# Performance work log

Hardware: AMD Instinct MI355X
Metric: run time of the kernel (lower is better)

Reference implementation:

```python
import jax, jax.numpy as jnp
import numpy as np

B, V, E, H, L = 1024, 8192, 64, 64, 16
TAU = 1.2
SOS_ID, EOS_ID = 1, 2


def setup_inputs() -> dict:
    key = jax.random.key(0)
    ks = jax.random.split(key, 7)
    hidden_state = jax.random.normal(ks[0], (B, H), dtype=jnp.float32)
    # embedding ~ N(0, 0.1) as in reset_parameters
    embedding = 0.1 * jax.random.normal(ks[1], (V, E), dtype=jnp.float32)
    # LSTMCell weight_ih: xavier uniform, weight_hh: orthogonal
    bound = float(np.sqrt(6.0 / (4 * H + E)))
    W_ih = jax.random.uniform(ks[2], (4 * H, E), minval=-bound, maxval=bound, dtype=jnp.float32)
    a = jax.random.normal(ks[3], (4 * H, H), dtype=jnp.float32)
    q, r = jnp.linalg.qr(a)
    W_hh = q * jnp.sign(jnp.diagonal(r))  # [4H, H] orthogonal columns
    b_ih = jnp.zeros((4 * H,), jnp.float32)
    b_hh = jnp.zeros((4 * H,), jnp.float32).at[H:2 * H].set(1.0)  # forget-gate bias = 1
    # linear_out is zero-init in the torch code; use small random values so the
    # math under test is non-trivial (init is data, not math).
    W_out = 0.02 * jax.random.normal(ks[4], (V, H), dtype=jnp.float32)
    b_out = jnp.zeros((V,), jnp.float32)
    # Precomputed standard Gumbel noise for deterministic sampling
    u = jax.random.uniform(ks[5], (L, B, V), minval=1e-10, maxval=1.0, dtype=jnp.float32)
    gumbels = -jnp.log(-jnp.log(u))
    return {
        'hidden_state': hidden_state, 'embedding': embedding,
        'W_ih': W_ih, 'W_hh': W_hh, 'b_ih': b_ih, 'b_hh': b_hh,
        'W_out': W_out, 'b_out': b_out, 'gumbels': gumbels,
    }


def reference(hidden_state, embedding, W_ih, W_hh, b_ih, b_hh, W_out, b_out, gumbels):
    b, h_dim = hidden_state.shape
    v = embedding.shape[0]
    n_steps = gumbels.shape[0]
    initial_length = n_steps + 1

    sos_onehot = jnp.zeros((b, v), hidden_state.dtype).at[:, SOS_ID].set(1.0)

    def step(carry, xs):
        h, c, prev_token, seq_lengths, ent = carry
        g, i = xs
        emb = prev_token @ embedding                                   # [b, E]
        gates = emb @ W_ih.T + b_ih + h @ W_hh.T + b_hh                # [b, 4H]
        ii, ff, gg, oo = jnp.split(gates, 4, axis=-1)                  # torch order i,f,g,o
        c = jax.nn.sigmoid(ff) * c + jax.nn.sigmoid(ii) * jnp.tanh(gg)
        h = jax.nn.sigmoid(oo) * jnp.tanh(c)
        logits = h @ W_out.T + b_out                                   # [b, V]
        logp = jax.nn.log_softmax(logits, axis=-1)
        p = jnp.exp(logp)
        ent = ent - jnp.sum(p * logp, axis=-1)
        # RelaxedOneHotCategorical rsample: softmax((log p + gumbel) / tau)
        y = jax.nn.softmax((logp + g) / TAU, axis=-1)
        y_hard = jax.nn.one_hot(jnp.argmax(y, axis=-1), v, dtype=y.dtype)
        token = jax.lax.stop_gradient(y_hard - y) + y                  # straight-through
        max_pred = jnp.max(token, axis=-1)
        vocab_idx = jnp.argmax(token, axis=-1)
        mask = (vocab_idx == EOS_ID) & (max_pred == 1.0) & (seq_lengths == initial_length)
        seq_lengths = jnp.where(mask, i + 2, seq_lengths)              # seq_pos + 1 with seq_pos = i+1
        return (h, c, token, seq_lengths, ent), (token, emb)

    c0 = jnp.zeros_like(hidden_state)
    seq0 = jnp.full((b,), initial_length, jnp.int32)
    ent0 = jnp.zeros((b,), hidden_state.dtype)
    (_, _, _, seq_lengths, ent), (tokens, embeds) = jax.lax.scan(
        step, (hidden_state, c0, sos_onehot, seq0, ent0),
        (gumbels, jnp.arange(n_steps, dtype=jnp.int32)))

    output = jnp.concatenate([sos_onehot[:, None, :], jnp.swapaxes(tokens, 0, 1)], axis=1)  # [b, L+1, V]
    embeds = jnp.swapaxes(embeds, 0, 1)                                                      # [b, L, E]
    entropy = jnp.mean(ent) / n_steps
    return output, seq_lengths, entropy, hidden_state, embeds
```

## Files before the change

kernel.cpp:

```cpp
#include <hip/hip_runtime.h>
#include <cmath>

#define B_ 1024
#define V_ 8192
#define E_ 64
#define H_ 64
#define L_ 16
#define SOS 1
#define EOS 2

typedef float f32x4 __attribute__((ext_vector_type(4)));

#define ONEHOT_OFF 0ull
#define SEQ_OFF    142606336ull
#define ENT_OFF    142607360ull
#define HID_OFF    142607361ull
#define EMB_OFF    142672897ull

__global__ __launch_bounds__(256) void init_zero_kernel(float* __restrict__ out)
{
    const int t = threadIdx.x;
    const int row = blockIdx.x;
    float* slab = out + ONEHOT_OFF + (size_t)row * (17 * 8192);
#pragma unroll
    for (int j = 0; j < 8; ++j) {
        f32x4 z = {0.f, 0.f, 0.f, 0.f};
        if (j == 0 && t == 0) z.y = 1.0f;
        __builtin_nontemporal_store(z, (f32x4*)(slab + j * 1024 + t * 4));
    }
    if (row == 0 && t == 1) out[ENT_OFF] = 0.f;
}

__global__ __launch_bounds__(256, 2) void logits_stats_kernel(
    const float* __restrict__ Wout, const float* __restrict__ bout,
    const float* __restrict__ gstep,
    const float* __restrict__ h,
    float* __restrict__ pm, float* __restrict__ pS, float* __restrict__ pT,
    float* __restrict__ pbv, int* __restrict__ pbi,
    float* __restrict__ out, int step)
{
    __shared__ float wV[256][64];
    __shared__ float hV[16][68];

    const int t  = threadIdx.x;
    const int rg = blockIdx.x >> 3;
    const int vs = blockIdx.x & 7;
    const int rowBase = rg * 16;
    const int tv = t & 63;
    const int tr = t >> 6;
    const int r0 = tr * 4;

    const int srow = t >> 4;
    const int scc  = t & 15;
    const int sdst = ((scc ^ srow) << 2);

    {
        const int rl = t >> 4;
        const int k0 = (t & 15) * 4;
        float4 hv = *(const float4*)(h + (size_t)(rowBase + rl) * 64 + k0);
        *(float4*)&hV[rl][k0] = hv;
    }

    {
        const f32x4 z = {0.f, 0.f, 0.f, 0.f};
        const size_t slab = ONEHOT_OFF + (size_t)(step + 1) * 8192 + (size_t)(vs * 1024 + t * 4);
#pragma unroll
        for (int r = 0; r < 16; ++r) {
            __builtin_nontemporal_store(z,
                (f32x4*)(out + (size_t)(rowBase + r) * (17 * 8192) + slab));
        }
    }

    float m[4], S[4], T[4], bv[4];
    int   bi[4];
#pragma unroll
    for (int r = 0; r < 4; ++r) {
        m[r] = -INFINITY; S[r] = 0.f; T[r] = 0.f; bv[r] = -INFINITY; bi[r] = 0;
    }

    for (int cc = 0; cc < 4; ++cc) {
        const int vglob = vs * 1024 + cc * 256;

        float gv[16], bo[4];
#pragma unroll
        for (int j = 0; j < 4; ++j) {
            const int v = vglob + 64 * j + tv;
            bo[j] = bout[v];
#pragma unroll
            for (int r = 0; r < 4; ++r)
                gv[j * 4 + r] = gstep[(size_t)(rowBase + r0 + r) * V_ + v];
        }

        __syncthreads();
#pragma unroll
        for (int j = 0; j < 16; ++j) {
            const int vl = srow + 16 * j;
            float4 w = *(const float4*)(Wout + (size_t)(vglob + vl) * 64 + scc * 4);
            *(float4*)&wV[vl][sdst] = w;
        }
        __syncthreads();

        float acc[4][4];
#pragma unroll
        for (int r = 0; r < 4; ++r)
#pragma unroll
            for (int j = 0; j < 4; ++j) acc[r][j] = 0.f;

#pragma unroll 4
        for (int k4 = 0; k4 < 16; ++k4) {
            const int ks = ((k4 ^ (tv & 15)) << 2);
            float4 wv[4], hv[4];
#pragma unroll
            for (int j = 0; j < 4; ++j) wv[j] = *(const float4*)&wV[tv + 64 * j][ks];
#pragma unroll
            for (int r = 0; r < 4; ++r) hv[r] = *(const float4*)&hV[r0 + r][k4 * 4];
#pragma unroll
            for (int r = 0; r < 4; ++r)
#pragma unroll
                for (int j = 0; j < 4; ++j)
                    acc[r][j] += hv[r].x * wv[j].x + hv[r].y * wv[j].y +
                                 hv[r].z * wv[j].z + hv[r].w * wv[j].w;
        }

#pragma unroll
        for (int j = 0; j < 4; ++j) {
            const int v  = vglob + 64 * j + tv;
#pragma unroll
            for (int r = 0; r < 4; ++r) {
                const float l = acc[r][j] + bo[j];
                const float s = l + gv[j * 4 + r];
                if (s > bv[r]) { bv[r] = s; bi[r] = v; }
                const float mn = fmaxf(m[r], l);
                const float e  = __expf(-fabsf(l - m[r]));
                const bool nw  = l > m[r];
                const float a  = nw ? e : 1.f;
                const float b2 = nw ? 1.f : e;
                S[r] = S[r] * a + b2;
                T[r] = T[r] * a + l * b2;
                m[r] = mn;
            }
        }
    }

#pragma unroll
    for (int off = 1; off < 64; off <<= 1) {
#pragma unroll
        for (int r = 0; r < 4; ++r) {
            const float mo  = __shfl_xor(m[r], off);
            const float So  = __shfl_xor(S[r], off);
            const float To  = __shfl_xor(T[r], off);
            const float bvo = __shfl_xor(bv[r], off);
            const int   bio = __shfl_xor(bi[r], off);
            const float mn = fmaxf(m[r], mo);
            const float ea = __expf(m[r] - mn);
            const float eb = __expf(mo - mn);
            S[r] = S[r] * ea + So * eb;
            T[r] = T[r] * ea + To * eb;
            m[r] = mn;
            if (bvo > bv[r] || (bvo == bv[r] && bio < bi[r])) { bv[r] = bvo; bi[r] = bio; }
        }
    }
    if (tv == 0) {
#pragma unroll
        for (int r = 0; r < 4; ++r) {
            const int row = rowBase + r0 + r;
            const int o = vs * 1024 + row;
            pm[o] = m[r]; pS[o] = S[r]; pT[o] = T[r]; pbv[o] = bv[r]; pbi[o] = bi[r];
        }
    }
}

__global__ __launch_bounds__(256) void combine_lstm_kernel(
    const float* __restrict__ emb_table,
    const float* __restrict__ W_ih, const float* __restrict__ W_hh,
    const float* __restrict__ b_ih, const float* __restrict__ b_hh,
    const float* __restrict__ hidden_in,
    float* __restrict__ h, float* __restrict__ c,
    float* __restrict__ ent, int* __restrict__ seq,
    const float* __restrict__ pm, const float* __restrict__ pS,
    const float* __restrict__ pT, const float* __restrict__ pbv,
    const int* __restrict__ pbi,
    float* __restrict__ out, int step)
{
    __shared__ float wrow[256][132];
    __shared__ float xcat[8][128];
    __shared__ float gatesL[8][256];
    __shared__ int   toksL[8];
    __shared__ float entL[8];

    const int t = threadIdx.x;
    const int rowBase = blockIdx.x * 8;

    if (step >= 0) {
        if (t < 8) {
            const int row = rowBase + t;
            float m = -INFINITY, S = 0.f, T = 0.f, bv = -INFINITY; int bi = 0;
            for (int s = 0; s < 8; ++s) {
                const int o = s * 1024 + row;
                const float ms = pm[o], Ss = pS[o], Ts = pT[o], bvs = pbv[o];
                const int bis = pbi[o];
                const float mn = fmaxf(m, ms);
                const float ea = __expf(m - mn), eb = __expf(ms - mn);
                S = S * ea + Ss * eb; T = T * ea + Ts * eb; m = mn;
                if (bvs > bv || (bvs == bv && bis < bi)) { bv = bvs; bi = bis; }
            }
            const float lse  = m + logf(S);
            const float entc = lse - T / S;
            const int tok = bi;
            out[ONEHOT_OFF + (size_t)row * (17 * 8192) + (size_t)(step + 1) * 8192 + tok] = 1.0f;
            const float ev = (step == 0) ? entc : (ent[row] + entc);
            ent[row] = ev;
            int sl = (step == 0) ? (L_ + 1) : seq[row];
            if (tok == EOS && sl == (L_ + 1)) sl = step + 2;
            seq[row] = sl;
            toksL[t] = tok;
            entL[t] = ev;
            if (step == 15) out[SEQ_OFF + row] = (float)sl;
        }
    } else {
        if (t < 8) toksL[t] = SOS;
    }
    __syncthreads();

    if (step == 15) {
        if (t == 0) {
            float a = 0.f;
            for (int r = 0; r < 8; ++r) a += entL[r];
            atomicAdd(out + ENT_OFF, a * (1.0f / (1024.0f * 16.0f)));
        }
        return;
    }

#pragma unroll
    for (int j = 0; j < 16; ++j) {
        const int f  = (t + 256 * j) * 4;
        const int gr = f >> 6;
        const int k0 = f & 63;
        *(float4*)&wrow[gr][k0]      = *(const float4*)(W_ih + f);
        *(float4*)&wrow[gr][64 + k0] = *(const float4*)(W_hh + f);
    }
    if (t < 128) {
        const int r = t >> 4, k0 = (t & 15) * 4;
        const int row = rowBase + r;
        const int tk = (step < 0) ? SOS : toksL[r];
        float4 evv = *(const float4*)(emb_table + (size_t)tk * 64 + k0);
        *(float4*)&xcat[r][k0] = evv;
        const size_t eo = EMB_OFF + ((size_t)row * 16 + (size_t)(step + 1)) * 64 + k0;
        out[eo + 0] = evv.x; out[eo + 1] = evv.y; out[eo + 2] = evv.z; out[eo + 3] = evv.w;
    } else {
        const int tt = t - 128;
        const int r = tt >> 4, k0 = (tt & 15) * 4;
        const int row = rowBase + r;
        const float* hsrc = (step < 0) ? (hidden_in + (size_t)row * 64 + k0)
                                       : (h + (size_t)row * 64 + k0);
        float4 hv = *(const float4*)hsrc;
        *(float4*)&xcat[r][64 + k0] = hv;
    }
    __syncthreads();

    {
        const float bia = b_ih[t] + b_hh[t];
        float acc[8];
#pragma unroll
        for (int r = 0; r < 8; ++r) acc[r] = bia;
        for (int k4 = 0; k4 < 32; ++k4) {
            const float4 w4 = *(const float4*)&wrow[t][k4 * 4];
#pragma unroll
            for (int r = 0; r < 8; ++r) {
                const float4 x4 = *(const float4*)&xcat[r][k4 * 4];
                acc[r] += x4.x * w4.x + x4.y * w4.y + x4.z * w4.z + x4.w * w4.w;
            }
        }
#pragma unroll
        for (int r = 0; r < 8; ++r) gatesL[r][t] = acc[r];
    }
    __syncthreads();

#pragma unroll
    for (int q = 0; q < 2; ++q) {
        const int u = t + q * 256;
        const int r = u >> 6, uu = u & 63;
        const int row = rowBase + r;
        const float ii = gatesL[r][uu];
        const float ff = gatesL[r][64 + uu];
        const float gg = gatesL[r][128 + uu];
        const float oo = gatesL[r][192 + uu];
        const float cp = (step < 0) ? 0.f : c[(size_t)row * 64 + uu];
        const float si = 1.f / (1.f + expf(-ii));
        const float sf = 1.f / (1.f + expf(-ff));
        const float so = 1.f / (1.f + expf(-oo));
        const float cn = sf * cp + si * tanhf(gg);
        const float hn = so * tanhf(cn);
        c[(size_t)row * 64 + uu] = cn;
        h[(size_t)row * 64 + uu] = hn;
    }
}

extern "C" void kernel_launch(void* const* d_in, const int* in_sizes, int n_in,
                              void* d_out, int out_size, void* d_ws, size_t ws_size,
                              hipStream_t stream) {
    (void)in_sizes; (void)ws_size; (void)out_size;
    if (n_in < 9) return;
    const float* hidden    = (const float*)d_in[0];
    const float* embedding = (const float*)d_in[1];
    const float* W_ih      = (const float*)d_in[2];
    const float* W_hh      = (const float*)d_in[3];
    const float* b_ih      = (const float*)d_in[4];
    const float* b_hh      = (const float*)d_in[5];
    const float* W_out     = (const float*)d_in[6];
    const float* b_out     = (const float*)d_in[7];
    const float* gumbels   = (const float*)d_in[8];
    float* out = (float*)d_out;

    float* wsf = (float*)d_ws;
    float* h   = wsf;
    float* c   = wsf + 65536;
    float* ent = wsf + 131072;
    int*   seq = (int*)(wsf + 132096);
    float* pm  = wsf + 133120;
    float* pS  = pm + 8192;
    float* pT  = pS + 8192;
    float* pbv = pT + 8192;
    int*   pbi = (int*)(pbv + 8192);

    (void)hipMemcpyAsync(out + HID_OFF, hidden, (size_t)B_ * H_ * sizeof(float),
                         hipMemcpyDeviceToDevice, stream);
    init_zero_kernel<<<1024, 256, 0, stream>>>(out);

    combine_lstm_kernel<<<128, 256, 0, stream>>>(embedding, W_ih, W_hh, b_ih, b_hh,
        hidden, h, c, ent, seq, pm, pS, pT, pbv, pbi, out, -1);
    for (int i = 0; i < 16; ++i) {
        logits_stats_kernel<<<512, 256, 0, stream>>>(W_out, b_out,
            gumbels + (size_t)i * B_ * V_, h, pm, pS, pT, pbv, pbi, out, i);
        combine_lstm_kernel<<<128, 256, 0, stream>>>(embedding, W_ih, W_hh, b_ih, b_hh,
            hidden, h, c, ent, seq, pm, pS, pT, pbv, pbi, out, i);
    }
}
```

Measured before the change: 1.543 ms.

## Fuse all decode steps into one persistent kernel with per-row-group flag barriers

Replaces the 33 per-step launches (logits/stats plus combine/LSTM) with a single persistent kernel of 512 blocks. The eight blocks covering a 16-row group synchronise through atomic flag counters in global memory. The LSTM gate computation is split across those eight blocks by hidden unit, with the cell state kept in registers and h exchanged through a workspace buffer. This removes launch gaps and the h/c round trips, but it depends on all 512 blocks being co-resident, since the spin barriers would deadlock otherwise, and it adds spin-wait overhead.

```diff
diff --git a/kernel.cpp b/kernel.cpp
--- a/kernel.cpp
+++ b/kernel.cpp
@@ -17,7 +17,8 @@
 #define HID_OFF    142607361ull
 #define EMB_OFF    142672897ull
 
-__global__ __launch_bounds__(256) void init_zero_kernel(float* __restrict__ out)
+__global__ __launch_bounds__(256) void init_zero_kernel(float* __restrict__ out,
+                                                        int* __restrict__ flags)
 {
     const int t = threadIdx.x;
     const int row = blockIdx.x;
@@ -29,18 +30,30 @@
         __builtin_nontemporal_store(z, (f32x4*)(slab + j * 1024 + t * 4));
     }
     if (row == 0 && t == 1) out[ENT_OFF] = 0.f;
+    if (row == 1) flags[t] = 0;
+    if (row == 2) flags[256 + t] = 0;
+    if (row == 3) flags[512 + t] = 0;
+    if (row == 4) flags[768 + t] = 0;
 }
 
-__global__ __launch_bounds__(256, 2) void logits_stats_kernel(
+__global__ __launch_bounds__(256, 2) void fused_kernel(
+    const float* __restrict__ emb_table,
+    const float* __restrict__ W_ih, const float* __restrict__ W_hh,
+    const float* __restrict__ b_ih, const float* __restrict__ b_hh,
+    const float* __restrict__ hidden_in,
     const float* __restrict__ Wout, const float* __restrict__ bout,
-    const float* __restrict__ gstep,
-    const float* __restrict__ h,
+    const float* __restrict__ gumbels,
     float* __restrict__ pm, float* __restrict__ pS, float* __restrict__ pT,
     float* __restrict__ pbv, int* __restrict__ pbi,
-    float* __restrict__ out, int step)
+    float* __restrict__ hx,
+    int* __restrict__ flags,
+    float* __restrict__ out)
 {
     __shared__ float wV[256][64];
-    __shared__ float hV[16][68];
+    __shared__ float X[16][132];
+    __shared__ int   tokL[16];
+    __shared__ float entL[16];
+    __shared__ int   seqL[16];
 
     const int t  = threadIdx.x;
     const int rg = blockIdx.x >> 3;
@@ -54,245 +67,249 @@
     const int scc  = t & 15;
     const int sdst = ((scc ^ srow) << 2);
 
+    float c_reg = 0.f;
+    int sync_ev = 0;
+
+    auto rg_sync = [&]() {
+        __syncthreads();
+        ++sync_ev;
+        if (t == 0) {
+            __hip_atomic_fetch_add(&flags[rg * 16], 1, __ATOMIC_RELEASE,
+                                   __HIP_MEMORY_SCOPE_AGENT);
+            while (__hip_atomic_load(&flags[rg * 16], __ATOMIC_ACQUIRE,
+                                     __HIP_MEMORY_SCOPE_AGENT) < 8 * sync_ev)
+                __builtin_amdgcn_s_sleep(2);
+        }
+        __syncthreads();
+    };
+
+    auto gates_lstm = [&]() {
+        float* Wg = &wV[0][0];
+#pragma unroll
+        for (int q = 0; q < 4; ++q) {
+            const int idx = (q * 256 + t) * 4;
+            const int gr = idx >> 7;
+            const int k  = idx & 127;
+            const int g = gr >> 3, ul = gr & 7;
+            const int wrow = g * 64 + vs * 8 + ul;
+            const float* src = (k < 64) ? (W_ih + (size_t)wrow * 64 + k)
+                                        : (W_hh + (size_t)wrow * 64 + (k - 64));
+            *(float4*)(Wg + gr * 128 + k) = *(const float4*)src;
+        }
+        __syncthreads();
+        if (t < 128) {
+            const int row = t >> 3, ul = t & 7;
+            const int unit = vs * 8 + ul;
+            float a0 = b_ih[unit]       + b_hh[unit];
+            float a1 = b_ih[64 + unit]  + b_hh[64 + unit];
+            float a2 = b_ih[128 + unit] + b_hh[128 + unit];
+            float a3 = b_ih[192 + unit] + b_hh[192 + unit];
+            for (int k4 = 0; k4 < 32; ++k4) {
+                const float4 x4 = *(const float4*)&X[row][k4 * 4];
+                const float4 w0 = *(const float4*)(Wg + (0 * 8 + ul) * 128 + k4 * 4);
+                const float4 w1 = *(const float4*)(Wg + (1 * 8 + ul) * 128 + k4 * 4);
+                const float4 w2 = *(const float4*)(Wg + (2 * 8 + ul) * 128 + k4 * 4);
+                const float4 w3 = *(const float4*)(Wg + (3 * 8 + ul) * 128 + k4 * 4);
+                a0 += x4.x * w0.x + x4.y * w0.y + x4.z * w0.z + x4.w * w0.w;
+                a1 += x4.x * w1.x + x4.y * w1.y + x4.z * w1.z + x4.w * w1.w;
+                a2 += x4.x * w2.x + x4.y * w2.y + x4.z * w2.z + x4.w * w2.w;
+                a3 += x4.x * w3.x + x4.y * w3.y + x4.z * w3.z + x4.w * w3.w;
+            }
+            const float si = 1.f / (1.f + expf(-a0));
+            const float sf = 1.f / (1.f + expf(-a1));
+            const float so = 1.f / (1.f + expf(-a3));
+            const float cn = sf * c_reg + si * tanhf(a2);
+            const float hn = so * tanhf(cn);
+            c_reg = cn;
+            hx[((size_t)(rg * 8 + vs) * 16 + row) * 8 + ul] = hn;
+        }
+        rg_sync();
+        {
+            const int row = t >> 4, k0 = (t & 15) * 4;
+            const int vsp = k0 >> 3, off = k0 & 7;
+            float4 hv = *(const float4*)(hx + ((size_t)(rg * 8 + vsp) * 16 + row) * 8 + off);
+            *(float4*)&X[row][64 + k0] = hv;
+        }
+        __syncthreads();
+    };
+
     {
-        const int rl = t >> 4;
-        const int k0 = (t & 15) * 4;
-        float4 hv = *(const float4*)(h + (size_t)(rowBase + rl) * 64 + k0);
-        *(float4*)&hV[rl][k0] = hv;
+        const int row = t >> 4, k0 = (t & 15) * 4;
+        float4 evv = *(const float4*)(emb_table + (size_t)SOS * 64 + k0);
+        *(float4*)&X[row][k0] = evv;
+        if (vs == 0) {
+            const size_t eo = EMB_OFF + ((size_t)(rowBase + row) * 16 + 0) * 64 + k0;
+            out[eo + 0] = evv.x; out[eo + 1] = evv.y; out[eo + 2] = evv.z; out[eo + 3] = evv.w;
+        }
+        float4 hv = *(const float4*)(hidden_in + (size_t)(rowBase + row) * 64 + k0);
+        *(float4*)&X[row][64 + k0] = hv;
     }
-
-    {
-        const f32x4 z = {0.f, 0.f, 0.f, 0.f};
-        const size_t slab = ONEHOT_OFF + (size_t)(step + 1) * 8192 + (size_t)(vs * 1024 + t * 4);
-#pragma unroll
-        for (int r = 0; r < 16; ++r) {
-            __builtin_nontemporal_store(z,
-                (f32x4*)(out + (size_t)(rowBase + r) * (17 * 8192) + slab));
-        }
-    }
-
-    float m[4], S[4], T[4], bv[4];
-    int   bi[4];
-#pragma unroll
-    for (int r = 0; r < 4; ++r) {
-        m[r] = -INFINITY; S[r] = 0.f; T[r] = 0.f; bv[r] = -INFINITY; bi[r] = 0;
-    }
-
-    for (int cc = 0; cc < 4; ++cc) {
-        const int vglob = vs * 1024 + cc * 256;
-
-        float gv[16], bo[4];
-#pragma unroll
-        for (int j = 0; j < 4; ++j) {
-            const int v = vglob + 64 * j + tv;
-            bo[j] = bout[v];
+    __syncthreads();
+    gates_lstm();
+
+    for (int i = 0; i < 16; ++i) {
+        const float* gstep = gumbels + (size_t)i * 8388608ull;
+
+        {
+            const f32x4 z = {0.f, 0.f, 0.f, 0.f};
+            const size_t slab = ONEHOT_OFF + (size_t)(i + 1) * 8192 + (size_t)(vs * 1024 + t * 4);
+#pragma unroll
+            for (int r = 0; r < 16; ++r) {
+                __builtin_nontemporal_store(z,
+                    (f32x4*)(out + (size_t)(rowBase + r) * (17 * 8192) + slab));
+            }
+        }
+
+        float m[4], S[4], T[4], bv[4];
+        int   bi[4];
+#pragma unroll
+        for (int r = 0; r < 4; ++r) {
+            m[r] = -INFINITY; S[r] = 0.f; T[r] = 0.f; bv[r] = -INFINITY; bi[r] = 0;
+        }
+
+        for (int cc = 0; cc < 4; ++cc) {
+            const int vglob = vs * 1024 + cc * 256;
+
+            float gv[16], bo[4];
+#pragma unroll
+            for (int j = 0; j < 4; ++j) {
+                const int v = vglob + 64 * j + tv;
+                bo[j] = bout[v];
+#pragma unroll
+                for (int r = 0; r < 4; ++r)
+                    gv[j * 4 + r] = gstep[(size_t)(rowBase + r0 + r) * V_ + v];
+            }
+
+            __syncthreads();
+#pragma unroll
+            for (int j = 0; j < 16; ++j) {
+                const int vl = srow + 16 * j;
+                float4 w = *(const float4*)(Wout + (size_t)(vglob + vl) * 64 + scc * 4);
+                *(float4*)&wV[vl][sdst] = w;
+            }
+            __syncthreads();
+
+            float acc[4][4];
 #pragma unroll
             for (int r = 0; r < 4; ++r)
-                gv[j * 4 + r] = gstep[(size_t)(rowBase + r0 + r) * V_ + v];
-        }
-
-        __syncthreads();
-#pragma unroll
-        for (int j = 0; j < 16; ++j) {
-            const int vl = srow + 16 * j;
-            float4 w = *(const float4*)(Wout + (size_t)(vglob + vl) * 64 + scc * 4);
-            *(float4*)&wV[vl][sdst] = w;
-        }
-        __syncthreads();
-
-        float acc[4][4];
-#pragma unroll
-        for (int r = 0; r < 4; ++r)
-#pragma unroll
-            for (int j = 0; j < 4; ++j) acc[r][j] = 0.f;
+#pragma unroll
+                for (int j = 0; j < 4; ++j) acc[r][j] = 0.f;
 
 #pragma unroll 4
-        for (int k4 = 0; k4 < 16; ++k4) {
-            const int ks = ((k4 ^ (tv & 15)) << 2);
-            float4 wv[4], hv[4];
-#pragma unroll
-            for (int j = 0; j < 4; ++j) wv[j] = *(const float4*)&wV[tv + 64 * j][ks];
-#pragma unroll
-            for (int r = 0; r < 4; ++r) hv[r] = *(const float4*)&hV[r0 + r][k4 * 4];
-#pragma unroll
-            for (int r = 0; r < 4; ++r)
-#pragma unroll
-                for (int j = 0; j < 4; ++j)
-                    acc[r][j] += hv[r].x * wv[j].x + hv[r].y * wv[j].y +
-                                 hv[r].z * wv[j].z + hv[r].w * wv[j].w;
-        }
-
-#pragma unroll
-        for (int j = 0; j < 4; ++j) {
-            const int v  = vglob + 64 * j + tv;
+            for (int k4 = 0; k4 < 16; ++k4) {
+                const int ks = ((k4 ^ (tv & 15)) << 2);
+                float4 wv[4], hv[4];
+#pragma unroll
+                for (int j = 0; j < 4; ++j) wv[j] = *(const float4*)&wV[tv + 64 * j][ks];
+#pragma unroll
+                for (int r = 0; r < 4; ++r) hv[r] = *(const float4*)&X[r0 + r][64 + k4 * 4];
+#pragma unroll
+                for (int r = 0; r < 4; ++r)
+#pragma unroll
+                    for (int j = 0; j < 4; ++j)
+                        acc[r][j] += hv[r].x * wv[j].x + hv[r].y * wv[j].y +
+                                     hv[r].z * wv[j].z + hv[r].w * wv[j].w;
+            }
+
+#pragma unroll
+            for (int j = 0; j < 4; ++j) {
+                const int v  = vglob + 64 * j + tv;
+#pragma unroll
+                for (int r = 0; r < 4; ++r) {
+                    const float l = acc[r][j] + bo[j];
+                    const float s = l + gv[j * 4 + r];
+                    if (s > bv[r]) { bv[r] = s; bi[r] = v; }
+                    const float mn = fmaxf(m[r], l);
+                    const float e  = __expf(-fabsf(l - m[r]));
+                    const bool nw  = l > m[r];
+                    const float a  = nw ? e : 1.f;
+                    const float b2 = nw ? 1.f : e;
+                    S[r] = S[r] * a + b2;
+                    T[r] = T[r] * a + l * b2;
+                    m[r] = mn;
+                }
+            }
+        }
+
+#pragma unroll
+        for (int off = 1; off < 64; off <<= 1) {
 #pragma unroll
             for (int r = 0; r < 4; ++r) {
-                const float l = acc[r][j] + bo[j];
-                const float s = l + gv[j * 4 + r];
-                if (s > bv[r]) { bv[r] = s; bi[r] = v; }
-                const float mn = fmaxf(m[r], l);
-                const float e  = __expf(-fabsf(l - m[r]));
-                const bool nw  = l > m[r];
-                const float a  = nw ? e : 1.f;
-                const float b2 = nw ? 1.f : e;
-                S[r] = S[r] * a + b2;
-                T[r] = T[r] * a + l * b2;
+                const float mo  = __shfl_xor(m[r], off);
+                const float So  = __shfl_xor(S[r], off);
+                const float To  = __shfl_xor(T[r], off);
+                const float bvo = __shfl_xor(bv[r], off);
+                const int   bio = __shfl_xor(bi[r], off);
+                const float mn = fmaxf(m[r], mo);
+                const float ea = __expf(m[r] - mn);
+                const float eb = __expf(mo - mn);
+                S[r] = S[r] * ea + So * eb;
+                T[r] = T[r] * ea + To * eb;
                 m[r] = mn;
-            }
-        }
-    }
-
-#pragma unroll
-    for (int off = 1; off < 64; off <<= 1) {
-#pragma unroll
-        for (int r = 0; r < 4; ++r) {
-            const float mo  = __shfl_xor(m[r], off);
-            const float So  = __shfl_xor(S[r], off);
-            const float To  = __shfl_xor(T[r], off);
-            const float bvo = __shfl_xor(bv[r], off);
-            const int   bio = __shfl_xor(bi[r], off);
-            const float mn = fmaxf(m[r], mo);
-            const float ea = __expf(m[r] - mn);
-            const float eb = __expf(mo - mn);
-            S[r] = S[r] * ea + So * eb;
-            T[r] = T[r] * ea + To * eb;
-            m[r] = mn;
-            if (bvo > bv[r] || (bvo == bv[r] && bio < bi[r])) { bv[r] = bvo; bi[r] = bio; }
-        }
-    }
-    if (tv == 0) {
-#pragma unroll
-        for (int r = 0; r < 4; ++r) {
-            const int row = rowBase + r0 + r;
-            const int o = vs * 1024 + row;
-            pm[o] = m[r]; pS[o] = S[r]; pT[o] = T[r]; pbv[o] = bv[r]; pbi[o] = bi[r];
-        }
-    }
-}
-
-__global__ __launch_bounds__(256) void combine_lstm_kernel(
-    const float* __restrict__ emb_table,
-    const float* __restrict__ W_ih, const float* __restrict__ W_hh,
-    const float* __restrict__ b_ih, const float* __restrict__ b_hh,
-    const float* __restrict__ hidden_in,
-    float* __restrict__ h, float* __restrict__ c,
-    float* __restrict__ ent, int* __restrict__ seq,
-    const float* __restrict__ pm, const float* __restrict__ pS,
-    const float* __restrict__ pT, const float* __restrict__ pbv,
-    const int* __restrict__ pbi,
-    float* __restrict__ out, int step)
-{
-    __shared__ float wrow[256][132];
-    __shared__ float xcat[8][128];
-    __shared__ float gatesL[8][256];
-    __shared__ int   toksL[8];
-    __shared__ float entL[8];
-
-    const int t = threadIdx.x;
-    const int rowBase = blockIdx.x * 8;
-
-    if (step >= 0) {
-        if (t < 8) {
+                if (bvo > bv[r] || (bvo == bv[r] && bio < bi[r])) { bv[r] = bvo; bi[r] = bio; }
+            }
+        }
+        if (tv == 0) {
+#pragma unroll
+            for (int r = 0; r < 4; ++r) {
+                const int row = rowBase + r0 + r;
+                const int o = vs * 1024 + row;
+                pm[o] = m[r]; pS[o] = S[r]; pT[o] = T[r]; pbv[o] = bv[r]; pbi[o] = bi[r];
+            }
+        }
+        rg_sync();
+
+        if (t < 16) {
             const int row = rowBase + t;
-            float m = -INFINITY, S = 0.f, T = 0.f, bv = -INFINITY; int bi = 0;
+            float m2 = -INFINITY, S2 = 0.f, T2 = 0.f, bv2 = -INFINITY; int bi2 = 0;
             for (int s = 0; s < 8; ++s) {
                 const int o = s * 1024 + row;
                 const float ms = pm[o], Ss = pS[o], Ts = pT[o], bvs = pbv[o];
                 const int bis = pbi[o];
-                const float mn = fmaxf(m, ms);
-                const float ea = __expf(m - mn), eb = __expf(ms - mn);
-                S = S * ea + Ss * eb; T = T * ea + Ts * eb; m = mn;
-                if (bvs > bv || (bvs == bv && bis < bi)) { bv = bvs; bi = bis; }
-            }
-            const float lse  = m + logf(S);
-            const float entc = lse - T / S;
-            const int tok = bi;
-            out[ONEHOT_OFF + (size_t)row * (17 * 8192) + (size_t)(step + 1) * 8192 + tok] = 1.0f;
-            const float ev = (step == 0) ? entc : (ent[row] + entc);
-            ent[row] = ev;
-            int sl = (step == 0) ? (L_ + 1) : seq[row];
-            if (tok == EOS && sl == (L_ + 1)) sl = step + 2;
-            seq[row] = sl;
-            toksL[t] = tok;
+                const float mn = fmaxf(m2, ms);
+                const float ea = __expf(m2 - mn), eb = __expf(ms - mn);
+                S2 = S2 * ea + Ss * eb; T2 = T2 * ea + Ts * eb; m2 = mn;
+                if (bvs > bv2 || (bvs == bv2 && bis < bi2)) { bv2 = bvs; bi2 = bis; }
+            }
+            const float lse  = m2 + logf(S2);
+            const float entc = lse - T2 / S2;
+            const int tok = bi2;
+            if (vs == 0)
+                out[ONEHOT_OFF + (size_t)row * (17 * 8192) + (size_t)(i + 1) * 8192 + tok] = 1.0f;
+            const float ev = (i == 0) ? entc : (entL[t] + entc);
             entL[t] = ev;
-            if (step == 15) out[SEQ_OFF + row] = (float)sl;
-        }
-    } else {
-        if (t < 8) toksL[t] = SOS;
-    }
-    __syncthreads();
-
-    if (step == 15) {
-        if (t == 0) {
-            float a = 0.f;
-            for (int r = 0; r < 8; ++r) a += entL[r];
-            atomicAdd(out + ENT_OFF, a * (1.0f / (1024.0f * 16.0f)));
-        }
-        return;
-    }
-
-#pragma unroll
-    for (int j = 0; j < 16; ++j) {
-        const int f  = (t + 256 * j) * 4;
-        const int gr = f >> 6;
-        const int k0 = f & 63;
-        *(float4*)&wrow[gr][k0]      = *(const float4*)(W_ih + f);
-        *(float4*)&wrow[gr][64 + k0] = *(const float4*)(W_hh + f);
-    }
-    if (t < 128) {
-        const int r = t >> 4, k0 = (t & 15) * 4;
-        const int row = rowBase + r;
-        const int tk = (step < 0) ? SOS : toksL[r];
-        float4 evv = *(const float4*)(emb_table + (size_t)tk * 64 + k0);
-        *(float4*)&xcat[r][k0] = evv;
-        const size_t eo = EMB_OFF + ((size_t)row * 16 + (size_t)(step + 1)) * 64 + k0;
-        out[eo + 0] = evv.x; out[eo + 1] = evv.y; out[eo + 2] = evv.z; out[eo + 3] = evv.w;
-    } else {
-        const int tt = t - 128;
-        const int r = tt >> 4, k0 = (tt & 15) * 4;
-        const int row = rowBase + r;
-        const float* hsrc = (step < 0) ? (hidden_in + (size_t)row * 64 + k0)
-                                       : (h + (size_t)row * 64 + k0);
-        float4 hv = *(const float4*)hsrc;
-        *(float4*)&xcat[r][64 + k0] = hv;
-    }
-    __syncthreads();
-
-    {
-        const float bia = b_ih[t] + b_hh[t];
-        float acc[8];
-#pragma unroll
-        for (int r = 0; r < 8; ++r) acc[r] = bia;
-        for (int k4 = 0; k4 < 32; ++k4) {
-            const float4 w4 = *(const float4*)&wrow[t][k4 * 4];
-#pragma unroll
-            for (int r = 0; r < 8; ++r) {
-                const float4 x4 = *(const float4*)&xcat[r][k4 * 4];
-                acc[r] += x4.x * w4.x + x4.y * w4.y + x4.z * w4.z + x4.w * w4.w;
-            }
-        }
-#pragma unroll
-        for (int r = 0; r < 8; ++r) gatesL[r][t] = acc[r];
-    }
-    __syncthreads();
-
-#pragma unroll
-    for (int q = 0; q < 2; ++q) {
-        const int u = t + q * 256;
-        const int r = u >> 6, uu = u & 63;
-        const int row = rowBase + r;
-        const float ii = gatesL[r][uu];
-        const float ff = gatesL[r][64 + uu];
-        const float gg = gatesL[r][128 + uu];
-        const float oo = gatesL[r][192 + uu];
-        const float cp = (step < 0) ? 0.f : c[(size_t)row * 64 + uu];
-        const float si = 1.f / (1.f + expf(-ii));
-        const float sf = 1.f / (1.f + expf(-ff));
-        const float so = 1.f / (1.f + expf(-oo));
-        const float cn = sf * cp + si * tanhf(gg);
-        const float hn = so * tanhf(cn);
-        c[(size_t)row * 64 + uu] = cn;
-        h[(size_t)row * 64 + uu] = hn;
+            int sl = (i == 0) ? (L_ + 1) : seqL[t];
+            if (tok == EOS && sl == (L_ + 1)) sl = i + 2;
+            seqL[t] = sl;
+            tokL[t] = tok;
+            if (i == 15 && vs == 0) out[SEQ_OFF + row] = (float)sl;
+        }
+        __syncthreads();
+
+        if (i == 15) {
+            if (vs == 0 && t == 0) {
+                float a = 0.f, b = 0.f;
+                for (int r = 0; r < 8; ++r)  a += entL[r];
+                for (int r = 8; r < 16; ++r) b += entL[r];
+                atomicAdd(out + ENT_OFF, a * (1.0f / (1024.0f * 16.0f)));
+                atomicAdd(out + ENT_OFF, b * (1.0f / (1024.0f * 16.0f)));
+            }
+            break;
+        }
+
+        {
+            const int row = t >> 4, k0 = (t & 15) * 4;
+            const int tk = tokL[row];
+            float4 evv = *(const float4*)(emb_table + (size_t)tk * 64 + k0);
+            *(float4*)&X[row][k0] = evv;
+            if (vs == 0) {
+                const size_t eo = EMB_OFF + ((size_t)(rowBase + row) * 16 + (size_t)(i + 1)) * 64 + k0;
+                out[eo + 0] = evv.x; out[eo + 1] = evv.y; out[eo + 2] = evv.z; out[eo + 3] = evv.w;
+            }
+        }
+        __syncthreads();
+
+        gates_lstm();
     }
 }
 
@@ -313,26 +330,18 @@
     float* out = (float*)d_out;
 
     float* wsf = (float*)d_ws;
-    float* h   = wsf;
-    float* c   = wsf + 65536;
-    float* ent = wsf + 131072;
-    int*   seq = (int*)(wsf + 132096);
-    float* pm  = wsf + 133120;
+    float* pm  = wsf;
     float* pS  = pm + 8192;
     float* pT  = pS + 8192;
     float* pbv = pT + 8192;
     int*   pbi = (int*)(pbv + 8192);
+    float* hx  = wsf + 40960;
+    int*   flags = (int*)(wsf + 40960 + 65536);
 
     (void)hipMemcpyAsync(out + HID_OFF, hidden, (size_t)B_ * H_ * sizeof(float),
                          hipMemcpyDeviceToDevice, stream);
-    init_zero_kernel<<<1024, 256, 0, stream>>>(out);
-
-    combine_lstm_kernel<<<128, 256, 0, stream>>>(embedding, W_ih, W_hh, b_ih, b_hh,
-        hidden, h, c, ent, seq, pm, pS, pT, pbv, pbi, out, -1);
-    for (int i = 0; i < 16; ++i) {
-        logits_stats_kernel<<<512, 256, 0, stream>>>(W_out, b_out,
-            gumbels + (size_t)i * B_ * V_, h, pm, pS, pT, pbv, pbi, out, i);
-        combine_lstm_kernel<<<128, 256, 0, stream>>>(embedding, W_ih, W_hh, b_ih, b_hh,
-            hidden, h, c, ent, seq, pm, pS, pT, pbv, pbi, out, i);
-    }
+    init_zero_kernel<<<1024, 256, 0, stream>>>(out, flags);
+
+    fused_kernel<<<512, 256, 0, stream>>>(embedding, W_ih, W_hh, b_ih, b_hh,
+        hidden, W_out, b_out, gumbels, pm, pS, pT, pbv, pbi, hx, flags, out);
 }
```

Result: slower. 2.509 ms (+62.6%).

## Fuse combine, LSTM cell and logits into one per-step kernel

Applied to the files above, without the earlier changes.

Merges the partial-stat combine, embedding lookup, LSTM cell and logits/softmax-stats work into a single step kernel, which removes the separate combine_lstm and init kernels and halves the number of launches per step. Each of the 8 vocab-slice blocks for a row group now recomputes that group's LSTM gates redundantly, reading W_ih/W_hh directly from global memory. h, c and the partial stats are double-buffered by step parity so no slice overwrites data other slices still read. Token and entropy history go to workspace and are reduced in a final small launch, and the one-hot zeroing is folded into step 0.

```diff
diff --git a/kernel.cpp b/kernel.cpp
--- a/kernel.cpp
+++ b/kernel.cpp
@@ -17,59 +17,181 @@
 #define HID_OFF    142607361ull
 #define EMB_OFF    142672897ull
 
-__global__ __launch_bounds__(256) void init_zero_kernel(float* __restrict__ out)
-{
-    const int t = threadIdx.x;
-    const int row = blockIdx.x;
-    float* slab = out + ONEHOT_OFF + (size_t)row * (17 * 8192);
-#pragma unroll
-    for (int j = 0; j < 8; ++j) {
-        f32x4 z = {0.f, 0.f, 0.f, 0.f};
-        if (j == 0 && t == 0) z.y = 1.0f;
-        __builtin_nontemporal_store(z, (f32x4*)(slab + j * 1024 + t * 4));
-    }
-    if (row == 0 && t == 1) out[ENT_OFF] = 0.f;
-}
-
-__global__ __launch_bounds__(256, 2) void logits_stats_kernel(
+__global__ __launch_bounds__(256, 2) void step_kernel(
+    const float* __restrict__ emb_table,
+    const float* __restrict__ W_ih, const float* __restrict__ W_hh,
+    const float* __restrict__ b_ih, const float* __restrict__ b_hh,
+    const float* __restrict__ hidden_in,
     const float* __restrict__ Wout, const float* __restrict__ bout,
-    const float* __restrict__ gstep,
-    const float* __restrict__ h,
+    const float* __restrict__ gumbels,
     float* __restrict__ pm, float* __restrict__ pS, float* __restrict__ pT,
     float* __restrict__ pbv, int* __restrict__ pbi,
+    float* __restrict__ h_ws, float* __restrict__ c_ws,
+    int* __restrict__ tok_ws, float* __restrict__ entc_ws,
     float* __restrict__ out, int step)
 {
     __shared__ float wV[256][64];
-    __shared__ float hV[16][68];
-
+    __shared__ float X[16][132];
+    __shared__ int   tokL[16];
+    __shared__ float entF[16];
+
+    const bool fin = (step == 16);
     const int t  = threadIdx.x;
-    const int rg = blockIdx.x >> 3;
-    const int vs = blockIdx.x & 7;
+    const int rg = fin ? (int)blockIdx.x : ((int)blockIdx.x >> 3);
+    const int vs = fin ? 0 : ((int)blockIdx.x & 7);
     const int rowBase = rg * 16;
     const int tv = t & 63;
     const int tr = t >> 6;
     const int r0 = tr * 4;
 
+    const int wp   = step & 1;
+    const int rpar = (step - 1) & 1;
+
     const int srow = t >> 4;
     const int scc  = t & 15;
     const int sdst = ((scc ^ srow) << 2);
 
+    if (!fin) {
+        const f32x4 z = {0.f, 0.f, 0.f, 0.f};
+        const size_t col = (size_t)(vs * 1024 + t * 4);
+#pragma unroll
+        for (int r = 0; r < 16; ++r) {
+            const size_t base = (size_t)(rowBase + r) * (17 * 8192);
+            __builtin_nontemporal_store(z,
+                (f32x4*)(out + base + (size_t)(step + 1) * 8192 + col));
+            if (step == 0)
+                __builtin_nontemporal_store(z, (f32x4*)(out + base + col));
+        }
+        if (step == 0 && blockIdx.x == 0 && t == 0) out[ENT_OFF] = 0.f;
+    }
+
+    if (step >= 1) {
+        if (t < 16) {
+            const int row = rowBase + t;
+            float m2 = -INFINITY, S2 = 0.f, T2 = 0.f, bv2 = -INFINITY; int bi2 = 0;
+            for (int s = 0; s < 8; ++s) {
+                const int o = rpar * 8192 + s * 1024 + row;
+                const float ms = pm[o], Ss = pS[o], Ts = pT[o], bvs = pbv[o];
+                const int bis = pbi[o];
+                const float mn = fmaxf(m2, ms);
+                const float ea = __expf(m2 - mn), eb = __expf(ms - mn);
+                S2 = S2 * ea + Ss * eb; T2 = T2 * ea + Ts * eb; m2 = mn;
+                if (bvs > bv2 || (bvs == bv2 && bis < bi2)) { bv2 = bvs; bi2 = bis; }
+            }
+            const float lse  = m2 + logf(S2);
+            const float entc = lse - T2 / S2;
+            const int tok = bi2;
+            if (vs == 0) {
+                out[ONEHOT_OFF + (size_t)row * (17 * 8192) + (size_t)step * 8192 + tok] = 1.0f;
+                tok_ws[(step - 1) * 1024 + row] = tok;
+                entc_ws[(step - 1) * 1024 + row] = entc;
+            }
+            tokL[t] = tok;
+            if (fin) {
+                float ev = entc_ws[0 * 1024 + row];
+                for (int s = 1; s < 15; ++s) ev += entc_ws[s * 1024 + row];
+                ev += entc;
+                int sl = L_ + 1;
+                for (int s = 0; s < 15; ++s) {
+                    const int tk = tok_ws[s * 1024 + row];
+                    if (tk == EOS && sl == (L_ + 1)) sl = s + 2;
+                }
+                if (tok == EOS && sl == (L_ + 1)) sl = 15 + 2;
+                out[SEQ_OFF + row] = (float)sl;
+                entF[t] = ev;
+            }
+        }
+    } else {
+        if (t < 16) tokL[t] = SOS;
+    }
+    __syncthreads();
+
+    if (step == 0 && vs == 0 && t < 16)
+        out[ONEHOT_OFF + (size_t)(rowBase + t) * (17 * 8192) + SOS] = 1.0f;
+
+    if (fin) {
+        if (t < 4) {
+            const float a = entF[4 * t] + entF[4 * t + 1] + entF[4 * t + 2] + entF[4 * t + 3];
+            atomicAdd(out + ENT_OFF, a * (1.0f / (1024.0f * 16.0f)));
+        }
+        return;
+    }
+
     {
-        const int rl = t >> 4;
-        const int k0 = (t & 15) * 4;
-        float4 hv = *(const float4*)(h + (size_t)(rowBase + rl) * 64 + k0);
-        *(float4*)&hV[rl][k0] = hv;
-    }
+        const int r = t >> 4, k0 = (t & 15) * 4;
+        const int row = rowBase + r;
+        const int tk = tokL[r];
+        float4 evv = *(const float4*)(emb_table + (size_t)tk * 64 + k0);
+        *(float4*)&X[r][k0] = evv;
+        if (vs == 0) {
+            const size_t eo = EMB_OFF + ((size_t)row * 16 + (size_t)step) * 64 + k0;
+            out[eo + 0] = evv.x; out[eo + 1] = evv.y; out[eo + 2] = evv.z; out[eo + 3] = evv.w;
+        }
+        const float* hsrc = (step == 0) ? (hidden_in + (size_t)row * 64 + k0)
+                                        : (h_ws + (size_t)rpar * 65536 + (size_t)row * 64 + k0);
+        float4 hv = *(const float4*)hsrc;
+        *(float4*)&X[r][64 + k0] = hv;
+    }
+    __syncthreads();
 
     {
-        const f32x4 z = {0.f, 0.f, 0.f, 0.f};
-        const size_t slab = ONEHOT_OFF + (size_t)(step + 1) * 8192 + (size_t)(vs * 1024 + t * 4);
-#pragma unroll
-        for (int r = 0; r < 16; ++r) {
-            __builtin_nontemporal_store(z,
-                (f32x4*)(out + (size_t)(rowBase + r) * (17 * 8192) + slab));
-        }
-    }
+        float* gw = &wV[0][0];
+        const int u = t;
+        const float bia = b_ih[u] + b_hh[u];
+        float acc[16];
+#pragma unroll
+        for (int r = 0; r < 16; ++r) acc[r] = bia;
+        const float* wih = W_ih + (size_t)u * 64;
+        const float* whh = W_hh + (size_t)u * 64;
+        for (int k4 = 0; k4 < 16; ++k4) {
+            const float4 w4 = *(const float4*)(wih + k4 * 4);
+#pragma unroll
+            for (int r = 0; r < 16; ++r) {
+                const float4 x4 = *(const float4*)&X[r][k4 * 4];
+                acc[r] += x4.x * w4.x + x4.y * w4.y + x4.z * w4.z + x4.w * w4.w;
+            }
+        }
+        for (int k4 = 0; k4 < 16; ++k4) {
+            const float4 w4 = *(const float4*)(whh + k4 * 4);
+#pragma unroll
+            for (int r = 0; r < 16; ++r) {
+                const float4 x4 = *(const float4*)&X[r][64 + k4 * 4];
+                acc[r] += x4.x * w4.x + x4.y * w4.y + x4.z * w4.z + x4.w * w4.w;
+            }
+        }
+#pragma unroll
+        for (int r = 0; r < 16; ++r) gw[r * 256 + u] = acc[r];
+    }
+    __syncthreads();
+
+    {
+        const float* gw = &wV[0][0];
+#pragma unroll
+        for (int q = 0; q < 4; ++q) {
+            const int lin = q * 256 + t;
+            const int r = lin >> 6, uu = lin & 63;
+            const int row = rowBase + r;
+            const float ii = gw[r * 256 + uu];
+            const float ff = gw[r * 256 + 64 + uu];
+            const float gg = gw[r * 256 + 128 + uu];
+            const float oo = gw[r * 256 + 192 + uu];
+            const float cp = (step == 0) ? 0.f
+                           : c_ws[(size_t)rpar * 65536 + (size_t)row * 64 + uu];
+            const float si = 1.f / (1.f + expf(-ii));
+            const float sf = 1.f / (1.f + expf(-ff));
+            const float so = 1.f / (1.f + expf(-oo));
+            const float cn = sf * cp + si * tanhf(gg);
+            const float hn = so * tanhf(cn);
+            X[r][64 + uu] = hn;
+            if (vs == 0) {
+                c_ws[(size_t)wp * 65536 + (size_t)row * 64 + uu] = cn;
+                h_ws[(size_t)wp * 65536 + (size_t)row * 64 + uu] = hn;
+            }
+        }
+    }
+    __syncthreads();
+
+    const float* gstep = gumbels + (size_t)step * 8388608ull;
 
     float m[4], S[4], T[4], bv[4];
     int   bi[4];
@@ -113,7 +235,7 @@
 #pragma unroll
             for (int j = 0; j < 4; ++j) wv[j] = *(const float4*)&wV[tv + 64 * j][ks];
 #pragma unroll
-            for (int r = 0; r < 4; ++r) hv[r] = *(const float4*)&hV[r0 + r][k4 * 4];
+            for (int r = 0; r < 4; ++r) hv[r] = *(const float4*)&X[r0 + r][64 + k4 * 4];
 #pragma unroll
             for (int r = 0; r < 4; ++r)
 #pragma unroll
@@ -164,135 +286,9 @@
 #pragma unroll
         for (int r = 0; r < 4; ++r) {
             const int row = rowBase + r0 + r;
-            const int o = vs * 1024 + row;
+            const int o = wp * 8192 + vs * 1024 + row;
             pm[o] = m[r]; pS[o] = S[r]; pT[o] = T[r]; pbv[o] = bv[r]; pbi[o] = bi[r];
         }
-    }
-}
-
-__global__ __launch_bounds__(256) void combine_lstm_kernel(
-    const float* __restrict__ emb_table,
-    const float* __restrict__ W_ih, const float* __restrict__ W_hh,
-    const float* __restrict__ b_ih, const float* __restrict__ b_hh,
-    const float* __restrict__ hidden_in,
-    float* __restrict__ h, float* __restrict__ c,
-    float* __restrict__ ent, int* __restrict__ seq,
-    const float* __restrict__ pm, const float* __restrict__ pS,
-    const float* __restrict__ pT, const float* __restrict__ pbv,
-    const int* __restrict__ pbi,
-    float* __restrict__ out, int step)
-{
-    __shared__ float wrow[256][132];
-    __shared__ float xcat[8][128];
-    __shared__ float gatesL[8][256];
-    __shared__ int   toksL[8];
-    __shared__ float entL[8];
-
-    const int t = threadIdx.x;
-    const int rowBase = blockIdx.x * 8;
-
-    if (step >= 0) {
-        if (t < 8) {
-            const int row = rowBase + t;
-            float m = -INFINITY, S = 0.f, T = 0.f, bv = -INFINITY; int bi = 0;
-            for (int s = 0; s < 8; ++s) {
-                const int o = s * 1024 + row;
-                const float ms = pm[o], Ss = pS[o], Ts = pT[o], bvs = pbv[o];
-                const int bis = pbi[o];
-                const float mn = fmaxf(m, ms);
-                const float ea = __expf(m - mn), eb = __expf(ms - mn);
-                S = S * ea + Ss * eb; T = T * ea + Ts * eb; m = mn;
-                if (bvs > bv || (bvs == bv && bis < bi)) { bv = bvs; bi = bis; }
-            }
-            const float lse  = m + logf(S);
-            const float entc = lse - T / S;
-            const int tok = bi;
-            out[ONEHOT_OFF + (size_t)row * (17 * 8192) + (size_t)(step + 1) * 8192 + tok] = 1.0f;
-            const float ev = (step == 0) ? entc : (ent[row] + entc);
-            ent[row] = ev;
-            int sl = (step == 0) ? (L_ + 1) : seq[row];
-            if (tok == EOS && sl == (L_ + 1)) sl = step + 2;
-            seq[row] = sl;
-            toksL[t] = tok;
-            entL[t] = ev;
-            if (step == 15) out[SEQ_OFF + row] = (float)sl;
-        }
-    } else {
-        if (t < 8) toksL[t] = SOS;
-    }
-    __syncthreads();
-
-    if (step == 15) {
-        if (t == 0) {
-            float a = 0.f;
-            for (int r = 0; r < 8; ++r) a += entL[r];
-            atomicAdd(out + ENT_OFF, a * (1.0f / (1024.0f * 16.0f)));
-        }
-        return;
-    }
-
-#pragma unroll
-    for (int j = 0; j < 16; ++j) {
-        const int f  = (t + 256 * j) * 4;
-        const int gr = f >> 6;
-        const int k0 = f & 63;
-        *(float4*)&wrow[gr][k0]      = *(const float4*)(W_ih + f);
-        *(float4*)&wrow[gr][64 + k0] = *(const float4*)(W_hh + f);
-    }
-    if (t < 128) {
-        const int r = t >> 4, k0 = (t & 15) * 4;
-        const int row = rowBase + r;
-        const int tk = (step < 0) ? SOS : toksL[r];
-        float4 evv = *(const float4*)(emb_table + (size_t)tk * 64 + k0);
-        *(float4*)&xcat[r][k0] = evv;
-        const size_t eo = EMB_OFF + ((size_t)row * 16 + (size_t)(step + 1)) * 64 + k0;
-        out[eo + 0] = evv.x; out[eo + 1] = evv.y; out[eo + 2] = evv.z; out[eo + 3] = evv.w;
-    } else {
-        const int tt = t - 128;
-        const int r = tt >> 4, k0 = (tt & 15) * 4;
-        const int row = rowBase + r;
-        const float* hsrc = (step < 0) ? (hidden_in + (size_t)row * 64 + k0)
-                                       : (h + (size_t)row * 64 + k0);
-        float4 hv = *(const float4*)hsrc;
-        *(float4*)&xcat[r][64 + k0] = hv;
-    }
-    __syncthreads();
-
-    {
-        const float bia = b_ih[t] + b_hh[t];
-        float acc[8];
-#pragma unroll
-        for (int r = 0; r < 8; ++r) acc[r] = bia;
-        for (int k4 = 0; k4 < 32; ++k4) {
-            const float4 w4 = *(const float4*)&wrow[t][k4 * 4];
-#pragma unroll
-            for (int r = 0; r < 8; ++r) {
-                const float4 x4 = *(const float4*)&xcat[r][k4 * 4];
-                acc[r] += x4.x * w4.x + x4.y * w4.y + x4.z * w4.z + x4.w * w4.w;
-            }
-        }
-#pragma unroll
-        for (int r = 0; r < 8; ++r) gatesL[r][t] = acc[r];
-    }
-    __syncthreads();
-
-#pragma unroll
-    for (int q = 0; q < 2; ++q) {
-        const int u = t + q * 256;
-        const int r = u >> 6, uu = u & 63;
-        const int row = rowBase + r;
-        const float ii = gatesL[r][uu];
-        const float ff = gatesL[r][64 + uu];
-        const float gg = gatesL[r][128 + uu];
-        const float oo = gatesL[r][192 + uu];
-        const float cp = (step < 0) ? 0.f : c[(size_t)row * 64 + uu];
-        const float si = 1.f / (1.f + expf(-ii));
-        const float sf = 1.f / (1.f + expf(-ff));
-        const float so = 1.f / (1.f + expf(-oo));
-        const float cn = sf * cp + si * tanhf(gg);
-        const float hn = so * tanhf(cn);
-        c[(size_t)row * 64 + uu] = cn;
-        h[(size_t)row * 64 + uu] = hn;
     }
 }
 
@@ -313,26 +309,24 @@
     float* out = (float*)d_out;
 
     float* wsf = (float*)d_ws;
-    float* h   = wsf;
-    float* c   = wsf + 65536;
-    float* ent = wsf + 131072;
-    int*   seq = (int*)(wsf + 132096);
-    float* pm  = wsf + 133120;
-    float* pS  = pm + 8192;
-    float* pT  = pS + 8192;
-    float* pbv = pT + 8192;
-    int*   pbi = (int*)(pbv + 8192);
+    float* pm   = wsf;
+    float* pS   = wsf + 16384;
+    float* pT   = wsf + 32768;
+    float* pbv  = wsf + 49152;
+    int*   pbi  = (int*)(wsf + 65536);
+    float* h_ws = wsf + 81920;
+    float* c_ws = wsf + 212992;
+    int*   tok_ws  = (int*)(wsf + 344064);
+    float* entc_ws = wsf + 360448;
 
     (void)hipMemcpyAsync(out + HID_OFF, hidden, (size_t)B_ * H_ * sizeof(float),
                          hipMemcpyDeviceToDevice, stream);
-    init_zero_kernel<<<1024, 256, 0, stream>>>(out);
-
-    combine_lstm_kernel<<<128, 256, 0, stream>>>(embedding, W_ih, W_hh, b_ih, b_hh,
-        hidden, h, c, ent, seq, pm, pS, pT, pbv, pbi, out, -1);
     for (int i = 0; i < 16; ++i) {
-        logits_stats_kernel<<<512, 256, 0, stream>>>(W_out, b_out,
-            gumbels + (size_t)i * B_ * V_, h, pm, pS, pT, pbv, pbi, out, i);
-        combine_lstm_kernel<<<128, 256, 0, stream>>>(embedding, W_ih, W_hh, b_ih, b_hh,
-            hidden, h, c, ent, seq, pm, pS, pT, pbv, pbi, out, i);
-    }
+        step_kernel<<<512, 256, 0, stream>>>(embedding, W_ih, W_hh, b_ih, b_hh,
+            hidden, W_out, b_out, gumbels, pm, pS, pT, pbv, pbi,
+            h_ws, c_ws, tok_ws, entc_ws, out, i);
+    }
+    step_kernel<<<64, 256, 0, stream>>>(embedding, W_ih, W_hh, b_ih, b_hh,
+        hidden, W_out, b_out, gumbels, pm, pS, pT, pbv, pbi,
+        h_ws, c_ws, tok_ws, entc_ws, out, 16);
 }
```

After: 1.622 ms. 5.1% more time.
